# Performance work log

Measured on AMD Instinct MI355X. Metric: run time of the kernel, lower is better.

Reference implementation:

```python
import jax, jax.numpy as jnp
import numpy as np


def _maxpool3d(x, win):
    # x: (B, C, D, H, W); SAME padding via w//2 on each spatial side, stride 1
    pads = [(0, 0), (0, 0)] + [(w // 2, w // 2) for w in win]
    return jax.lax.reduce_window(x, -jnp.inf, jax.lax.max,
                                 (1, 1) + tuple(win), (1, 1, 1, 1, 1), pads)


def _soft_skeletonize(x, thresh_width=5):
    # Iterative morphological erosion: x <- relu(x - relu(maxpool(minpool(x)) - minpool(x)))
    for _ in range(thresh_width):
        p1 = -_maxpool3d(-x, (3, 1, 1))  # directional min-pool along D
        p2 = -_maxpool3d(-x, (1, 3, 1))  # along H
        p3 = -_maxpool3d(-x, (1, 1, 3))  # along W
        min_pool = jnp.minimum(jnp.minimum(p1, p2), p3)
        contour = jax.nn.relu(_maxpool3d(min_pool, (3, 3, 3)) - min_pool)
        x = jax.nn.relu(x - contour)
    return x


def _positive_intersection(center_line, vessel):
    B, C = center_line.shape[0], center_line.shape[1]
    clf = center_line.reshape(B, C, -1)
    vf = vessel.reshape(B, C, -1)
    intersection = jnp.sum(clf * vf, axis=-1).sum(0)          # (C,)
    return (intersection + 1e-12) / (jnp.sum(clf, axis=-1).sum(0) + 1e-12)


def setup_inputs() -> dict:
    key = jax.random.key(0)
    k1, k2 = jax.random.split(key)
    B, C, D, H, W = 2, 1, 64, 256, 256
    logits = jax.random.normal(k1, (B, C, D, H, W), dtype=jnp.float32)
    target = jax.random.uniform(k2, (B, C, D, H, W), dtype=jnp.float32)
    mask = jnp.ones((B, C, D, H, W), dtype=jnp.float32)
    return {"logits": logits, "target": target, "mask": mask}


def reference(logits, target, mask):
    THRESH_WIDTH = 5
    pred = jax.nn.sigmoid(logits) * mask
    tgt = target * mask
    target_skeleton = _soft_skeletonize(tgt, THRESH_WIDTH)
    cl_pred = _soft_skeletonize(pred, THRESH_WIDTH)
    clrecall = _positive_intersection(target_skeleton, pred)[0]
    clacc = _positive_intersection(cl_pred, tgt)[0]
    cldice = 2.0 * clrecall * clacc / (clrecall + clacc + 1e-12)
    return 1.0 - cldice
```

## Files before the change

kernel.cpp:

```cpp
#include <hip/hip_runtime.h>
#include <math.h>


constexpr int Bn = 2;
constexpr int D  = 64;
constexpr int H  = 256;
constexpr int W  = 256;
constexpr int HW = H * W;
constexpr int NV = Bn * D * H * W;

constexpr int CD  = 16;
constexpr int XSF = 76;
constexpr int RSF = 68;

__device__ __forceinline__ void lds_barrier() {
    asm volatile("s_waitcnt lgkmcnt(0)" ::: "memory");
    __builtin_amdgcn_s_barrier();
    asm volatile("" ::: "memory");
}

__device__ __forceinline__ float4 vmin4(float4 a, float4 b) {
    return make_float4(fminf(a.x,b.x), fminf(a.y,b.y), fminf(a.z,b.z), fminf(a.w,b.w));
}
__device__ __forceinline__ float4 vmax4(float4 a, float4 b) {
    return make_float4(fmaxf(a.x,b.x), fmaxf(a.y,b.y), fmaxf(a.z,b.z), fmaxf(a.w,b.w));
}
__device__ __forceinline__ float4 sh1(float4 a, float4 b) { return make_float4(a.y,a.z,a.w,b.x); }
__device__ __forceinline__ float4 sh3(float4 a, float4 b) { return make_float4(a.w,b.x,b.y,b.z); }

__global__ __launch_bounds__(256) void prep_kernel(const float* __restrict__ logits,
                                                   const float* __restrict__ target,
                                                   const float* __restrict__ mask,
                                                   float* __restrict__ pred,
                                                   float* __restrict__ tgt) {
    int i = (blockIdx.x * 256 + threadIdx.x) * 4;
    float4 lg = *(const float4*)(logits + i);
    float4 tg = *(const float4*)(target + i);
    float4 mk = *(const float4*)(mask + i);
    float4 p, t;
    p.x = (1.0f/(1.0f+expf(-lg.x)))*mk.x;  t.x = tg.x*mk.x;
    p.y = (1.0f/(1.0f+expf(-lg.y)))*mk.y;  t.y = tg.y*mk.y;
    p.z = (1.0f/(1.0f+expf(-lg.z)))*mk.z;  t.z = tg.z*mk.z;
    p.w = (1.0f/(1.0f+expf(-lg.w)))*mk.w;  t.w = tg.w*mk.w;
    *(float4*)(pred + i) = p;
    *(float4*)(tgt + i)  = t;
}

template <bool FINAL>
__global__ __launch_bounds__(256) void skel_iter_kernel(
        const float* __restrict__ in0, float* __restrict__ out0,
        const float* __restrict__ oth0, double* __restrict__ acc0,
        const float* __restrict__ in1, float* __restrict__ out1,
        const float* __restrict__ oth1, double* __restrict__ acc1) {
    __shared__ float sx[4][36 * XSF];
    __shared__ float srm[2][34 * RSF];

    int cpx = gridDim.x >> 3;
    int hwb = blockIdx.x;
    int bx  = (hwb & 7) * cpx + (hwb >> 3);

    int t   = bx >> 8;
    int bt  = bx & 255;
    int w0  = (bt & 3) * 64;
    int h0  = ((bt >> 2) & 7) * 32;
    int gd0 = ((bt >> 5) & 3) * CD;
    int b   = (bt >> 7) & 1;

    const float* xin  = t ? in1  : in0;
    float*       xout = t ? out1 : out0;
    const float* oth  = t ? oth1 : oth0;
    double*      accp = t ? acc1 : acc0;

    int tid = threadIdx.x;
    int r   = tid >> 3;
    int k   = tid & 7;

    const float* xb  = xin + b * (D * HW);
    float*       ob  = xout ? (xout + b * (D * HW)) : nullptr;
    const float* otb = oth + b * (D * HW);

    const float4 INF4  = make_float4( INFINITY,  INFINITY,  INFINITY,  INFINITY);
    const float4 NINF4 = make_float4(-INFINITY, -INFINITY, -INFINITY, -INFINITY);

    int j1 = tid + 256, j2 = tid + 512;
    int sr0 = tid / 18, sq0 = tid - sr0 * 18;
    int sr1 = j1 / 18,  sq1 = j1 - sr1 * 18;
    int sr2 = j2 / 18,  sq2 = j2 - sr2 * 18;
    bool has2 = (j2 < 648);

    float4 Pa, Pb, Pc;
    auto issue = [&](int p) {
        if (p < 0 || p >= D) { Pa = Pb = Pc = INF4; return; }
        const float* pl = xb + p * HW;
        auto f = [&](int row, int qd) -> float4 {
            int gh = h0 - 2 + row;
            int gw = w0 - 4 + 4 * qd;
            if ((unsigned)gh < (unsigned)H && (unsigned)gw < (unsigned)W)
                return *(const float4*)(pl + gh * W + gw);
            return INF4;
        };
        Pa = f(sr0, sq0);
        Pb = f(sr1, sq1);
        Pc = has2 ? f(sr2, sq2) : INF4;
    };
    auto commitv = [&](int p, float4 va, float4 vb, float4 vc) {
        float* dst = sx[(p + 4) & 3];
        *(float4*)&dst[sr0 * XSF + 4 * sq0] = va;
        *(float4*)&dst[sr1 * XSF + 4 * sq1] = vb;
        if (has2) *(float4*)&dst[sr2 * XSF + 4 * sq2] = vc;
    };

    issue(gd0 - 2); commitv(gd0 - 2, Pa, Pb, Pc);
    issue(gd0 - 1); commitv(gd0 - 1, Pa, Pb, Pc);
    issue(gd0);     commitv(gd0,     Pa, Pb, Pc);
    issue(gd0 + 1);
    __syncthreads();

    float4 h1lo=NINF4, h1hi=NINF4, h2lo=NINF4, h2hi=NINF4;
    float4 p1lo=NINF4, p1hi=NINF4, p2lo=NINF4, p2hi=NINF4;
    float4 rmplo=NINF4, rmphi=NINF4;
    float4 xplo=INF4, xphi=INF4;
    double s0 = 0.0, s1 = 0.0;

    for (int s = gd0 - 1; s <= gd0 + CD + 1; ++s) {
        float4 Ta = Pa, Tb = Pb, Tc = Pc;
        if (s + 3 <= gd0 + CD + 1) issue(s + 3);
        if (s + 2 <= gd0 + CD + 1) commitv(s + 2, Ta, Tb, Tc);

        bool sv = (s >= 0 && s < D && s <= gd0 + CD);
        float4 lo = NINF4, hi = NINF4, rmlo = NINF4, rmhi = NINF4;
        if (sv) {
            const float* xq = sx[(s + 4) & 3];
            const float* xm = sx[(s + 3) & 3];
            const float* xp = sx[(s + 5) & 3];
            {
                const float* rc  = &xq[(r + 2) * XSF + 8 * k];
                const float* ru  = &xq[(r + 1) * XSF + 8 * k];
                const float* rd  = &xq[(r + 3) * XSF + 8 * k];
                const float* rm_ = &xm[(r + 2) * XSF + 8 * k];
                const float* rp_ = &xp[(r + 2) * XSF + 8 * k];
                float4 X0 = *(const float4*)rc,        X1 = *(const float4*)(rc + 4),
                       X2 = *(const float4*)(rc + 8),  X3 = *(const float4*)(rc + 12);
                float4 U1 = *(const float4*)(ru + 4),  U2 = *(const float4*)(ru + 8);
                float4 Dn1= *(const float4*)(rd + 4),  Dn2= *(const float4*)(rd + 8);
                float4 M1 = *(const float4*)(rm_ + 4), M2 = *(const float4*)(rm_ + 8);
                float4 P1 = *(const float4*)(rp_ + 4), P2 = *(const float4*)(rp_ + 8);
                lo = vmin4(vmin4(sh3(X0, X1), X1), sh1(X1, X2));
                lo = vmin4(lo, vmin4(vmin4(U1, Dn1), vmin4(M1, P1)));
                hi = vmin4(vmin4(sh3(X1, X2), X2), sh1(X2, X3));
                hi = vmin4(hi, vmin4(vmin4(U2, Dn2), vmin4(M2, P2)));
                float eL = __shfl_up(hi.w, 1);
                float eR = __shfl_down(lo.x, 1);
                if (k == 0) {
                    eL = -INFINITY;
                    if (w0 > 0) {
                        float w3 = fminf(fminf(X0.z, X0.w), X1.x);
                        eL = fminf(fminf(w3, fminf(ru[3], rd[3])),
                                   fminf(rm_[3], rp_[3]));
                    }
                }
                if (k == 7) {
                    eR = -INFINITY;
                    if (w0 + 64 < W) {
                        float w3 = fminf(fminf(X2.w, X3.x), X3.y);
                        eR = fminf(fminf(w3, fminf(ru[12], rd[12])),
                                   fminf(rm_[12], rp_[12]));
                    }
                }
                rmlo = vmax4(vmax4(make_float4(eL, lo.x, lo.y, lo.z), lo),
                             make_float4(lo.y, lo.z, lo.w, hi.x));
                rmhi = vmax4(vmax4(make_float4(lo.w, hi.x, hi.y, hi.z), hi),
                             make_float4(hi.y, hi.z, hi.w, eR));
                float* rw = &srm[s & 1][(r + 1) * RSF + 8 * k];
                *(float4*)rw       = rmlo;
                *(float4*)(rw + 4) = rmhi;
            }
            if (tid < 16) {
                int mr2 = (tid >> 3) ? 33 : 0;
                int k2  = tid & 7;
                int gh2 = h0 - 1 + mr2;
                float4 hlo = NINF4, hhi = NINF4;
                if ((unsigned)gh2 < (unsigned)H) {
                    int xr2 = mr2 + 1;
                    const float* rc  = &xq[xr2 * XSF + 8 * k2];
                    const float* ru  = &xq[(xr2 - 1) * XSF + 8 * k2];
                    const float* rd  = &xq[(xr2 + 1) * XSF + 8 * k2];
                    const float* rm_ = &xm[xr2 * XSF + 8 * k2];
                    const float* rp_ = &xp[xr2 * XSF + 8 * k2];
                    float4 X0 = *(const float4*)rc,        X1 = *(const float4*)(rc + 4),
                           X2 = *(const float4*)(rc + 8),  X3 = *(const float4*)(rc + 12);
                    float4 U1 = *(const float4*)(ru + 4),  U2 = *(const float4*)(ru + 8);
                    float4 Dn1= *(const float4*)(rd + 4),  Dn2= *(const float4*)(rd + 8);
                    float4 M1 = *(const float4*)(rm_ + 4), M2 = *(const float4*)(rm_ + 8);
                    float4 P1 = *(const float4*)(rp_ + 4), P2 = *(const float4*)(rp_ + 8);
                    float4 l2 = vmin4(vmin4(sh3(X0, X1), X1), sh1(X1, X2));
                    l2 = vmin4(l2, vmin4(vmin4(U1, Dn1), vmin4(M1, P1)));
                    float4 g2 = vmin4(vmin4(sh3(X1, X2), X2), sh1(X2, X3));
                    g2 = vmin4(g2, vmin4(vmin4(U2, Dn2), vmin4(M2, P2)));
                    float eL2 = -INFINITY, eR2 = -INFINITY;
                    if (w0 + 8 * k2 - 1 >= 0) {
                        float w3 = fminf(fminf(X0.z, X0.w), X1.x);
                        eL2 = fminf(fminf(w3, fminf(ru[3], rd[3])),
                                    fminf(rm_[3], rp_[3]));
                    }
                    if (w0 + 8 * k2 + 8 < W) {
                        float w3 = fminf(fminf(X2.w, X3.x), X3.y);
                        eR2 = fminf(fminf(w3, fminf(ru[12], rd[12])),
                                    fminf(rm_[12], rp_[12]));
                    }
                    hlo = vmax4(vmax4(make_float4(eL2, l2.x, l2.y, l2.z), l2),
                                make_float4(l2.y, l2.z, l2.w, g2.x));
                    hhi = vmax4(vmax4(make_float4(l2.w, g2.x, g2.y, g2.z), g2),
                                make_float4(g2.y, g2.z, g2.w, eR2));
                }
                float* hw = &srm[s & 1][mr2 * RSF + 8 * k2];
                *(float4*)hw       = hlo;
                *(float4*)(hw + 4) = hhi;
            }
        }

        int dm = s - 1;
        float4 xclo = INF4, xchi = INF4;
        if (dm >= gd0 && dm <= gd0 + CD - 1) {
            const float* xd = sx[(dm + 4) & 3];
            xclo = *(const float4*)&xd[(r + 2) * XSF + 8 * k + 4];
            xchi = *(const float4*)&xd[(r + 2) * XSF + 8 * k + 8];
        }

        float4 hclo = NINF4, hchi = NINF4;
        if (s >= gd0 && dm >= 0 && dm < D) {
            const float* m = srm[dm & 1];
            float4 a0 = *(const float4*)&m[r * RSF + 8 * k];
            float4 a1 = *(const float4*)&m[r * RSF + 8 * k + 4];
            float4 b0 = *(const float4*)&m[(r + 2) * RSF + 8 * k];
            float4 b1 = *(const float4*)&m[(r + 2) * RSF + 8 * k + 4];
            hclo = vmax4(vmax4(a0, rmplo), b0);
            hchi = vmax4(vmax4(a1, rmphi), b1);
        }

        int d = s - 2;
        if (d >= gd0 && d <= gd0 + CD - 1) {
            float4 mxlo = vmax4(h2lo, vmax4(h1lo, hclo));
            float4 mxhi = vmax4(h2hi, vmax4(h1hi, hchi));
            float4 rlo, rhi;
            rlo.x = fmaxf(xplo.x - (mxlo.x - p2lo.x), 0.0f);
            rlo.y = fmaxf(xplo.y - (mxlo.y - p2lo.y), 0.0f);
            rlo.z = fmaxf(xplo.z - (mxlo.z - p2lo.z), 0.0f);
            rlo.w = fmaxf(xplo.w - (mxlo.w - p2lo.w), 0.0f);
            rhi.x = fmaxf(xphi.x - (mxhi.x - p2hi.x), 0.0f);
            rhi.y = fmaxf(xphi.y - (mxhi.y - p2hi.y), 0.0f);
            rhi.z = fmaxf(xphi.z - (mxhi.z - p2hi.z), 0.0f);
            rhi.w = fmaxf(xphi.w - (mxhi.w - p2hi.w), 0.0f);
            long off = (long)d * HW + (h0 + r) * W + (w0 + 8 * k);
            if constexpr (FINAL) {
                float4 o1 = *(const float4*)(otb + off);
                float4 o2 = *(const float4*)(otb + off + 4);
                s0 += (double)(rlo.x * o1.x) + (double)(rlo.y * o1.y)
                    + (double)(rlo.z * o1.z) + (double)(rlo.w * o1.w)
                    + (double)(rhi.x * o2.x) + (double)(rhi.y * o2.y)
                    + (double)(rhi.z * o2.z) + (double)(rhi.w * o2.w);
                s1 += (double)rlo.x + (double)rlo.y + (double)rlo.z + (double)rlo.w
                    + (double)rhi.x + (double)rhi.y + (double)rhi.z + (double)rhi.w;
            } else {
                *(float4*)(ob + off)     = rlo;
                *(float4*)(ob + off + 4) = rhi;
            }
        }

        h2lo = h1lo; h2hi = h1hi; h1lo = hclo; h1hi = hchi;
        p2lo = p1lo; p2hi = p1hi; p1lo = lo;   p1hi = hi;
        rmplo = rmlo; rmphi = rmhi;
        xplo = xclo;  xphi = xchi;

        lds_barrier();
    }

    if constexpr (FINAL) {
        for (int off = 32; off > 0; off >>= 1) {
            s0 += __shfl_down(s0, off, 64);
            s1 += __shfl_down(s1, off, 64);
        }
        if ((tid & 63) == 0) {
            atomicAdd(&accp[0], s0);
            atomicAdd(&accp[1], s1);
        }
    }
}

__global__ void final_kernel(const double* __restrict__ acc, float* __restrict__ out) {
    double clrecall = (acc[0] + 1e-12) / (acc[1] + 1e-12);
    double clacc    = (acc[2] + 1e-12) / (acc[3] + 1e-12);
    double cldice   = 2.0 * clrecall * clacc / (clrecall + clacc + 1e-12);
    out[0] = (float)(1.0 - cldice);
}

extern "C" void kernel_launch(void* const* d_in, const int* in_sizes, int n_in,
                              void* d_out, int out_size, void* d_ws, size_t ws_size,
                              hipStream_t stream) {
    const float* logits = (const float*)d_in[0];
    const float* target = (const float*)d_in[1];
    const float* mask   = (const float*)d_in[2];
    float* out = (float*)d_out;

    float* pred = (float*)d_ws;
    float* tgt  = pred + NV;
    float* A0   = tgt + NV;
    float* B0   = A0 + NV;

    bool big = ws_size >= (size_t)6 * NV * 4 + 64;
    float* A1   = big ? (B0 + NV) : A0;
    float* B1   = big ? (A1 + NV) : B0;
    double* acc = big ? (double*)(B1 + NV) : (double*)(B0 + NV);

    hipMemsetAsync(acc, 0, 4 * sizeof(double), stream);

    dim3 blk(256);
    prep_kernel<<<dim3(NV / 1024), blk, 0, stream>>>(logits, target, mask, pred, tgt);

    if (big) {
        dim3 g(512);
        skel_iter_kernel<false><<<g, blk, 0, stream>>>(tgt, A0, pred, acc, pred, A1, tgt, acc + 2);
        skel_iter_kernel<false><<<g, blk, 0, stream>>>(A0, B0, pred, acc, A1, B1, tgt, acc + 2);
        skel_iter_kernel<false><<<g, blk, 0, stream>>>(B0, A0, pred, acc, B1, A1, tgt, acc + 2);
        skel_iter_kernel<false><<<g, blk, 0, stream>>>(A0, B0, pred, acc, A1, B1, tgt, acc + 2);
        skel_iter_kernel<true ><<<g, blk, 0, stream>>>(B0, nullptr, pred, acc, B1, nullptr, tgt, acc + 2);
    } else {
        dim3 g(256);
        skel_iter_kernel<false><<<g, blk, 0, stream>>>(tgt, A0, pred, acc, tgt, A0, pred, acc);
        skel_iter_kernel<false><<<g, blk, 0, stream>>>(A0, B0, pred, acc, A0, B0, pred, acc);
        skel_iter_kernel<false><<<g, blk, 0, stream>>>(B0, A0, pred, acc, B0, A0, pred, acc);
        skel_iter_kernel<false><<<g, blk, 0, stream>>>(A0, B0, pred, acc, A0, B0, pred, acc);
        skel_iter_kernel<true ><<<g, blk, 0, stream>>>(B0, nullptr, pred, acc, B0, nullptr, pred, acc);
        skel_iter_kernel<false><<<g, blk, 0, stream>>>(pred, A0, tgt, acc + 2, pred, A0, tgt, acc + 2);
        skel_iter_kernel<false><<<g, blk, 0, stream>>>(A0, B0, tgt, acc + 2, A0, B0, tgt, acc + 2);
        skel_iter_kernel<false><<<g, blk, 0, stream>>>(B0, A0, tgt, acc + 2, B0, A0, tgt, acc + 2);
        skel_iter_kernel<false><<<g, blk, 0, stream>>>(A0, B0, tgt, acc + 2, A0, B0, tgt, acc + 2);
        skel_iter_kernel<true ><<<g, blk, 0, stream>>>(B0, nullptr, tgt, acc + 2, B0, nullptr, tgt, acc + 2);
    }

    final_kernel<<<1, 1, 0, stream>>>(acc, out);
}
```

Baseline: 314.0 us.

## Stage halo planes via direct global-to-LDS loads with vmcnt-gated barriers

Replaces the register-staged prefetch (load float4s into registers, then write them to LDS) with `global_load_lds` DMA straight into a ring of four LDS plane slots. Out-of-range halo elements are read from a small buffer of infinities that the prep kernel writes. The per-plane barrier now waits only on the older outstanding vector-memory ops, so the next plane can stream in while the current one is computed. It also reuses the already-loaded previous-plane registers as the centre value, saving an LDS read. The aim is fewer VGPRs and LDS write instructions plus deeper load overlap. The risk is that the vmcnt(2) accounting is fragile: each plane issues three loads, and stores may interleave.

```diff
diff --git a/kernel.cpp b/kernel.cpp
--- a/kernel.cpp
+++ b/kernel.cpp
@@ -11,10 +11,16 @@
 
 constexpr int CD  = 16;
 constexpr int XSF = 76;
+constexpr int XPQ = 768;
 constexpr int RSF = 68;
 
-__device__ __forceinline__ void lds_barrier() {
-    asm volatile("s_waitcnt lgkmcnt(0)" ::: "memory");
+__device__ __forceinline__ void seg_barrier_v0() {
+    asm volatile("s_waitcnt vmcnt(0) lgkmcnt(0)" ::: "memory");
+    __builtin_amdgcn_s_barrier();
+    asm volatile("" ::: "memory");
+}
+__device__ __forceinline__ void seg_barrier_v2() {
+    asm volatile("s_waitcnt vmcnt(2) lgkmcnt(0)" ::: "memory");
     __builtin_amdgcn_s_barrier();
     asm volatile("" ::: "memory");
 }
@@ -32,7 +38,8 @@
                                                    const float* __restrict__ target,
                                                    const float* __restrict__ mask,
                                                    float* __restrict__ pred,
-                                                   float* __restrict__ tgt) {
+                                                   float* __restrict__ tgt,
+                                                   float* __restrict__ infbuf) {
     int i = (blockIdx.x * 256 + threadIdx.x) * 4;
     float4 lg = *(const float4*)(logits + i);
     float4 tg = *(const float4*)(target + i);
@@ -44,6 +51,9 @@
     p.w = (1.0f/(1.0f+expf(-lg.w)))*mk.w;  t.w = tg.w*mk.w;
     *(float4*)(pred + i) = p;
     *(float4*)(tgt + i)  = t;
+    if (blockIdx.x == 0 && threadIdx.x == 0) {
+        *(float4*)infbuf = make_float4(INFINITY, INFINITY, INFINITY, INFINITY);
+    }
 }
 
 template <bool FINAL>
@@ -51,8 +61,9 @@
         const float* __restrict__ in0, float* __restrict__ out0,
         const float* __restrict__ oth0, double* __restrict__ acc0,
         const float* __restrict__ in1, float* __restrict__ out1,
-        const float* __restrict__ oth1, double* __restrict__ acc1) {
-    __shared__ float sx[4][36 * XSF];
+        const float* __restrict__ oth1, double* __restrict__ acc1,
+        const float* __restrict__ infbuf) {
+    __shared__ float sx[4][XPQ * 4];
     __shared__ float srm[2][34 * RSF];
 
     int cpx = gridDim.x >> 3;
@@ -71,9 +82,11 @@
     const float* oth  = t ? oth1 : oth0;
     double*      accp = t ? acc1 : acc0;
 
-    int tid = threadIdx.x;
-    int r   = tid >> 3;
-    int k   = tid & 7;
+    int tid  = threadIdx.x;
+    int r    = tid >> 3;
+    int k    = tid & 7;
+    int wv   = tid >> 6;
+    int lane = tid & 63;
 
     const float* xb  = xin + b * (D * HW);
     float*       ob  = xout ? (xout + b * (D * HW)) : nullptr;
@@ -82,38 +95,35 @@
     const float4 INF4  = make_float4( INFINITY,  INFINITY,  INFINITY,  INFINITY);
     const float4 NINF4 = make_float4(-INFINITY, -INFINITY, -INFINITY, -INFINITY);
 
-    int j1 = tid + 256, j2 = tid + 512;
-    int sr0 = tid / 18, sq0 = tid - sr0 * 18;
-    int sr1 = j1 / 18,  sq1 = j1 - sr1 * 18;
-    int sr2 = j2 / 18,  sq2 = j2 - sr2 * 18;
-    bool has2 = (j2 < 648);
-
-    float4 Pa, Pb, Pc;
-    auto issue = [&](int p) {
-        if (p < 0 || p >= D) { Pa = Pb = Pc = INF4; return; }
-        const float* pl = xb + p * HW;
-        auto f = [&](int row, int qd) -> float4 {
-            int gh = h0 - 2 + row;
-            int gw = w0 - 4 + 4 * qd;
-            if ((unsigned)gh < (unsigned)H && (unsigned)gw < (unsigned)W)
-                return *(const float4*)(pl + gh * W + gw);
-            return INF4;
-        };
-        Pa = f(sr0, sq0);
-        Pb = f(sr1, sq1);
-        Pc = has2 ? f(sr2, sq2) : INF4;
+    int  offe[3];
+    bool okl[3];
+    for (int i = 0; i < 3; ++i) {
+        int c = wv + 4 * i;
+        int j = 64 * c + lane;
+        int row = j / 19;
+        int q = j - 19 * row;
+        int gh = h0 - 2 + row;
+        int gw = w0 - 4 + 4 * q;
+        okl[i] = (q < 18) && (row < 36) &&
+                 ((unsigned)gh < (unsigned)H) && ((unsigned)gw < (unsigned)W);
+        offe[i] = gh * W + gw;
+    }
+
+    auto issue_g = [&](int p) {
+        bool pok = (p >= 0 && p < D);
+        const float* pbase = xb + (long)p * HW;
+        float* slot = sx[(p + 4) & 3];
+        #pragma unroll
+        for (int i = 0; i < 3; ++i) {
+            const float* src = (pok && okl[i]) ? (pbase + offe[i]) : infbuf;
+            float* dst = slot + (wv + 4 * i) * 256;
+            __builtin_amdgcn_global_load_lds(
+                (const __attribute__((address_space(1))) void*)src,
+                (__attribute__((address_space(3))) void*)dst, 16, 0, 0);
+        }
     };
-    auto commitv = [&](int p, float4 va, float4 vb, float4 vc) {
-        float* dst = sx[(p + 4) & 3];
-        *(float4*)&dst[sr0 * XSF + 4 * sq0] = va;
-        *(float4*)&dst[sr1 * XSF + 4 * sq1] = vb;
-        if (has2) *(float4*)&dst[sr2 * XSF + 4 * sq2] = vc;
-    };
-
-    issue(gd0 - 2); commitv(gd0 - 2, Pa, Pb, Pc);
-    issue(gd0 - 1); commitv(gd0 - 1, Pa, Pb, Pc);
-    issue(gd0);     commitv(gd0,     Pa, Pb, Pc);
-    issue(gd0 + 1);
+
+    issue_g(gd0 - 2); issue_g(gd0 - 1); issue_g(gd0); issue_g(gd0 + 1);
     __syncthreads();
 
     float4 h1lo=NINF4, h1hi=NINF4, h2lo=NINF4, h2hi=NINF4;
@@ -123,12 +133,12 @@
     double s0 = 0.0, s1 = 0.0;
 
     for (int s = gd0 - 1; s <= gd0 + CD + 1; ++s) {
-        float4 Ta = Pa, Tb = Pb, Tc = Pc;
-        if (s + 3 <= gd0 + CD + 1) issue(s + 3);
-        if (s + 2 <= gd0 + CD + 1) commitv(s + 2, Ta, Tb, Tc);
+        if (s >= gd0 && s + 2 <= gd0 + CD + 1) issue_g(s + 2);
+        asm volatile("" ::: "memory");
 
         bool sv = (s >= 0 && s < D && s <= gd0 + CD);
         float4 lo = NINF4, hi = NINF4, rmlo = NINF4, rmhi = NINF4;
+        float4 vM1 = INF4, vM2 = INF4;
         if (sv) {
             const float* xq = sx[(s + 4) & 3];
             const float* xm = sx[(s + 3) & 3];
@@ -145,6 +155,7 @@
                 float4 Dn1= *(const float4*)(rd + 4),  Dn2= *(const float4*)(rd + 8);
                 float4 M1 = *(const float4*)(rm_ + 4), M2 = *(const float4*)(rm_ + 8);
                 float4 P1 = *(const float4*)(rp_ + 4), P2 = *(const float4*)(rp_ + 8);
+                vM1 = M1; vM2 = M2;
                 lo = vmin4(vmin4(sh3(X0, X1), X1), sh1(X1, X2));
                 lo = vmin4(lo, vmin4(vmin4(U1, Dn1), vmin4(M1, P1)));
                 hi = vmin4(vmin4(sh3(X1, X2), X2), sh1(X2, X3));
@@ -222,9 +233,12 @@
         int dm = s - 1;
         float4 xclo = INF4, xchi = INF4;
         if (dm >= gd0 && dm <= gd0 + CD - 1) {
-            const float* xd = sx[(dm + 4) & 3];
-            xclo = *(const float4*)&xd[(r + 2) * XSF + 8 * k + 4];
-            xchi = *(const float4*)&xd[(r + 2) * XSF + 8 * k + 8];
+            if (sv) { xclo = vM1; xchi = vM2; }
+            else {
+                const float* xd = sx[(dm + 4) & 3];
+                xclo = *(const float4*)&xd[(r + 2) * XSF + 8 * k + 4];
+                xchi = *(const float4*)&xd[(r + 2) * XSF + 8 * k + 8];
+            }
         }
 
         float4 hclo = NINF4, hchi = NINF4;
@@ -272,7 +286,8 @@
         rmplo = rmlo; rmphi = rmhi;
         xplo = xclo;  xphi = xchi;
 
-        lds_barrier();
+        if (s <= gd0 + 1) seg_barrier_v0();
+        else              seg_barrier_v2();
     }
 
     if constexpr (FINAL) {
@@ -308,34 +323,35 @@
     float* B0   = A0 + NV;
 
     bool big = ws_size >= (size_t)6 * NV * 4 + 64;
-    float* A1   = big ? (B0 + NV) : A0;
-    float* B1   = big ? (A1 + NV) : B0;
-    double* acc = big ? (double*)(B1 + NV) : (double*)(B0 + NV);
+    float* A1    = big ? (B0 + NV) : A0;
+    float* B1    = big ? (A1 + NV) : B0;
+    double* acc  = big ? (double*)(B1 + NV) : (double*)(B0 + NV);
+    float* infb  = (float*)(acc + 4);
 
     hipMemsetAsync(acc, 0, 4 * sizeof(double), stream);
 
     dim3 blk(256);
-    prep_kernel<<<dim3(NV / 1024), blk, 0, stream>>>(logits, target, mask, pred, tgt);
+    prep_kernel<<<dim3(NV / 1024), blk, 0, stream>>>(logits, target, mask, pred, tgt, infb);
 
     if (big) {
         dim3 g(512);
-        skel_iter_kernel<false><<<g, blk, 0, stream>>>(tgt, A0, pred, acc, pred, A1, tgt, acc + 2);
-        skel_iter_kernel<false><<<g, blk, 0, stream>>>(A0, B0, pred, acc, A1, B1, tgt, acc + 2);
-        skel_iter_kernel<false><<<g, blk, 0, stream>>>(B0, A0, pred, acc, B1, A1, tgt, acc + 2);
-        skel_iter_kernel<false><<<g, blk, 0, stream>>>(A0, B0, pred, acc, A1, B1, tgt, acc + 2);
-        skel_iter_kernel<true ><<<g, blk, 0, stream>>>(B0, nullptr, pred, acc, B1, nullptr, tgt, acc + 2);
+        skel_iter_kernel<false><<<g, blk, 0, stream>>>(tgt, A0, pred, acc, pred, A1, tgt, acc + 2, infb);
+        skel_iter_kernel<false><<<g, blk, 0, stream>>>(A0, B0, pred, acc, A1, B1, tgt, acc + 2, infb);
+        skel_iter_kernel<false><<<g, blk, 0, stream>>>(B0, A0, pred, acc, B1, A1, tgt, acc + 2, infb);
+        skel_iter_kernel<false><<<g, blk, 0, stream>>>(A0, B0, pred, acc, A1, B1, tgt, acc + 2, infb);
+        skel_iter_kernel<true ><<<g, blk, 0, stream>>>(B0, nullptr, pred, acc, B1, nullptr, tgt, acc + 2, infb);
     } else {
         dim3 g(256);
-        skel_iter_kernel<false><<<g, blk, 0, stream>>>(tgt, A0, pred, acc, tgt, A0, pred, acc);
-        skel_iter_kernel<false><<<g, blk, 0, stream>>>(A0, B0, pred, acc, A0, B0, pred, acc);
-        skel_iter_kernel<false><<<g, blk, 0, stream>>>(B0, A0, pred, acc, B0, A0, pred, acc);
-        skel_iter_kernel<false><<<g, blk, 0, stream>>>(A0, B0, pred, acc, A0, B0, pred, acc);
-        skel_iter_kernel<true ><<<g, blk, 0, stream>>>(B0, nullptr, pred, acc, B0, nullptr, pred, acc);
-        skel_iter_kernel<false><<<g, blk, 0, stream>>>(pred, A0, tgt, acc + 2, pred, A0, tgt, acc + 2);
-        skel_iter_kernel<false><<<g, blk, 0, stream>>>(A0, B0, tgt, acc + 2, A0, B0, tgt, acc + 2);
-        skel_iter_kernel<false><<<g, blk, 0, stream>>>(B0, A0, tgt, acc + 2, B0, A0, tgt, acc + 2);
-        skel_iter_kernel<false><<<g, blk, 0, stream>>>(A0, B0, tgt, acc + 2, A0, B0, tgt, acc + 2);
-        skel_iter_kernel<true ><<<g, blk, 0, stream>>>(B0, nullptr, tgt, acc + 2, B0, nullptr, tgt, acc + 2);
+        skel_iter_kernel<false><<<g, blk, 0, stream>>>(tgt, A0, pred, acc, tgt, A0, pred, acc, infb);
+        skel_iter_kernel<false><<<g, blk, 0, stream>>>(A0, B0, pred, acc, A0, B0, pred, acc, infb);
+        skel_iter_kernel<false><<<g, blk, 0, stream>>>(B0, A0, pred, acc, B0, A0, pred, acc, infb);
+        skel_iter_kernel<false><<<g, blk, 0, stream>>>(A0, B0, pred, acc, A0, B0, pred, acc, infb);
+        skel_iter_kernel<true ><<<g, blk, 0, stream>>>(B0, nullptr, pred, acc, B0, nullptr, pred, acc, infb);
+        skel_iter_kernel<false><<<g, blk, 0, stream>>>(pred, A0, tgt, acc + 2, pred, A0, tgt, acc + 2, infb);
+        skel_iter_kernel<false><<<g, blk, 0, stream>>>(A0, B0, tgt, acc + 2, A0, B0, tgt, acc + 2, infb);
+        skel_iter_kernel<false><<<g, blk, 0, stream>>>(B0, A0, tgt, acc + 2, B0, A0, tgt, acc + 2, infb);
+        skel_iter_kernel<false><<<g, blk, 0, stream>>>(A0, B0, tgt, acc + 2, A0, B0, tgt, acc + 2, infb);
+        skel_iter_kernel<true ><<<g, blk, 0, stream>>>(B0, nullptr, tgt, acc + 2, B0, nullptr, tgt, acc + 2, infb);
     }
 
     final_kernel<<<1, 1, 0, stream>>>(acc, out);
```

New measurement: 282.7 us. 1.11x faster.
